# Kernel optimization log

Measured on AMD Instinct MI355X. Metric: run time of the kernel, lower is better.

The kernel has to match this reference:

```python
import jax, jax.numpy as jnp
import numpy as np

EPS = 1e-12  # matches torch F.normalize default eps
KERNEL_NUM = 128
SUPPORT_NUM = 7


def _knn_exclude_self(x, k):
    # x: (bs, n, d) -> (bs, n, k) indices of k nearest neighbors (self excluded)
    inner = jnp.einsum('bnd,bmd->bnm', x, x)
    q = jnp.sum(x * x, axis=2)
    dist = -2.0 * inner + q[:, None, :] + q[:, :, None]
    _, idx = jax.lax.top_k(-dist, k + 1)  # smallest distances
    return idx[:, :, 1:]


def _gather_neighbors(t, idx):
    # t: (bs, n, c), idx: (bs, n, k) -> (bs, n, k, c)
    return jax.vmap(lambda tb, ib: tb[ib])(t, idx)


def setup_inputs() -> dict:
    key = jax.random.key(0)
    k1, k2, k3, k4 = jax.random.split(key, 4)
    bs, n = 2, 8192
    stdv = 1.0 / np.sqrt(SUPPORT_NUM * KERNEL_NUM)
    return {
        'vertices': jax.random.normal(k1, (bs, n, 3), dtype=jnp.float32),
        'directions': jax.random.uniform(k2, (3, SUPPORT_NUM * KERNEL_NUM), dtype=jnp.float32, minval=-stdv, maxval=stdv),
        'W_ste': jax.random.normal(k3, (KERNEL_NUM, 3), dtype=jnp.float32) * (1.0 / np.sqrt(3.0)),
        'W_conv2': jax.random.normal(k4, (KERNEL_NUM, 2 * KERNEL_NUM), dtype=jnp.float32) * (1.0 / np.sqrt(2.0 * KERNEL_NUM)),
        'neighbor_num': 16,
    }


def reference(vertices, directions, W_ste, W_conv2, neighbor_num):
    bs, n, _ = vertices.shape
    kernel_num = W_ste.shape[0]
    support_num = directions.shape[1] // kernel_num

    # STE branch: 1x1 conv over channels (3 -> kernel_num)
    f_ste = jnp.einsum('bnd,kd->bnk', vertices, W_ste)

    # receptive fields (RF-P): kNN in point space, normalized directions
    idx = _knn_exclude_self(vertices, neighbor_num)  # (bs, n, K)
    nbrs = _gather_neighbors(vertices, idx)          # (bs, n, K, 3)
    dirvec = nbrs - vertices[:, :, None, :]
    dir_norm = dirvec / jnp.maximum(jnp.linalg.norm(dirvec, axis=-1, keepdims=True), EPS)

    # graph conv
    sup = directions / jnp.maximum(jnp.linalg.norm(directions, axis=0, keepdims=True), EPS)
    theta = jax.nn.relu(jnp.einsum('bnkd,ds->bnks', dir_norm, sup))
    theta = theta.reshape(bs, n, neighbor_num, support_num, kernel_num)
    feature = jnp.mean(jnp.max(theta, axis=2), axis=2)  # (bs, n, kernel_num)

    # ORL: global pooling over kNN-maxed features (same point-space kNN indices)
    nb_feat = jnp.max(_gather_neighbors(feature, idx), axis=2)   # (bs, n, kernel_num)
    f_global = jnp.broadcast_to(jnp.mean(nb_feat, axis=1, keepdims=True), feature.shape)
    feat_cat = jnp.concatenate([feature, f_global], axis=-1)     # (bs, n, 2*kernel_num)
    feature = jnp.einsum('bnc,kc->bnk', feat_cat, W_conv2) + feature

    return feature + f_ste
```

## Files before the change

kernel.cpp:

```cpp
#include <hip/hip_runtime.h>
#include <math.h>

#define N     8192
#define BS    2
#define KNN   16
#define SUP   7
#define KC    128
#define SK    (SUP*KC)
#define NCH   32
#define CH    (N/NCH)
#define SLOTS 12
#define CAP   (NCH*SLOTS)
#define QG    256
#define PPB   16
#define OPB   8
#define LCAP  96
#define LSTR  98

typedef unsigned long long ull;
typedef unsigned short ushort4v __attribute__((ext_vector_type(4)));

__device__ __forceinline__ float dist2(float4 a, float4 b) {
    float dx = a.x - b.x, dy = a.y - b.y, dz = a.z - b.z;
    return fmaf(dx, dx, fmaf(dy, dy, dz * dz));
}

#define SW(Kt) { ull _lo = (Kt < _n) ? Kt : _n; ull _hi = (Kt < _n) ? _n : Kt; Kt = _lo; _n = _hi; }
#define INS16(NK) do { ull _n = (NK); if (_n < K15) { \
    SW(K0) SW(K1) SW(K2) SW(K3) SW(K4) SW(K5) SW(K6) SW(K7) \
    SW(K8) SW(K9) SW(K10) SW(K11) SW(K12) SW(K13) SW(K14) SW(K15) } } while(0)

#define DECL16 ull K0=~0ull,K1=~0ull,K2=~0ull,K3=~0ull,K4=~0ull,K5=~0ull,K6=~0ull,K7=~0ull, \
                   K8=~0ull,K9=~0ull,K10=~0ull,K11=~0ull,K12=~0ull,K13=~0ull,K14=~0ull,K15=~0ull;

__global__ void k_prep(const float* __restrict__ verts, const float* __restrict__ dirs,
                       const float* __restrict__ wste, const float* __restrict__ wconv,
                       float4* __restrict__ vb4, float4* __restrict__ sup4,
                       float4* __restrict__ wste4, float4* __restrict__ wt4) {
    int t = blockIdx.x * blockDim.x + threadIdx.x;
    if (t < BS * N) {
        float x = verts[t*3], y = verts[t*3+1], z = verts[t*3+2];
        vb4[t] = make_float4(x, y, z, 0.5f * fmaf(x, x, fmaf(y, y, z*z)));
    }
    int u = t - BS * N;
    if (u >= 0 && u < SK) {
        float x = dirs[u], y = dirs[SK + u], z = dirs[2*SK + u];
        float inv = 1.f / fmaxf(sqrtf(fmaf(x, x, fmaf(y, y, z*z))), 1e-12f);
        sup4[u] = make_float4(x*inv, y*inv, z*inv, 0.f);
    }
    int v = u - SK;
    if (v >= 0 && v < KC)
        wste4[v] = make_float4(wste[v*3], wste[v*3+1], wste[v*3+2], 0.f);
    int w = v - KC;
    if (w >= 0 && w < 32*KC) {
        int c4 = w >> 7, k = w & 127;
        const float* r = wconv + k*2*KC + c4*4;
        wt4[w] = make_float4(r[0], r[1], r[2], r[3]);
    }
}

__global__ void k_thr(const float4* __restrict__ vb4, float* __restrict__ thr) {
    __shared__ float4 SB[2048];
    __shared__ float4 SA[512];
    int b = blockIdx.y;
    int tid = threadIdx.x;
    const float4* vb = vb4 + b * N;
#pragma unroll
    for (int s = 0; s < 8; ++s)
        SB[tid + 256*s] = vb[tid + 256*s];
    __syncthreads();
#pragma unroll
    for (int s = 0; s < 2; ++s) {
        int t = tid + 256*s;
        SA[t] = SB[4*t];
    }
    __syncthreads();
    int sub = tid & 7;
    int i = blockIdx.x * 32 + (tid >> 3);
    float4 q = vb[i];
    float b0 = 3.4e38f, b1 = 3.4e38f, b2 = 3.4e38f, b3 = 3.4e38f;
#pragma unroll 8
    for (int s = 0; s < 64; ++s) {
        int t = s * 8 + sub;
        float d = dist2(q, SA[t]);
        if (4*t == i) d = 3.4e38f;
        float t0 = fminf(b0, d); float r = fmaxf(b0, d); b0 = t0;
        float t1 = fminf(b1, r); r = fmaxf(b1, r); b1 = t1;
        float t2 = fminf(b2, r); r = fmaxf(b2, r); b2 = t2;
        b3 = fminf(b3, r);
    }
#pragma unroll
    for (int st = 1; st < 8; st <<= 1) {
        float c0 = __shfl_xor(b0, st, 64);
        float c1 = __shfl_xor(b1, st, 64);
        float c2 = __shfl_xor(b2, st, 64);
        float c3 = __shfl_xor(b3, st, 64);
        float m0 = fminf(b0, c3), m1 = fminf(b1, c2);
        float m2 = fminf(b2, c1), m3 = fminf(b3, c0);
        float x0 = fminf(m0, m2), x2 = fmaxf(m0, m2);
        float x1 = fminf(m1, m3), x3 = fmaxf(m1, m3);
        b0 = fminf(x0, x1); b1 = fmaxf(x0, x1);
        b2 = fminf(x2, x3); b3 = fmaxf(x2, x3);
    }
    float t4 = b3;
    int c = 0;
#pragma unroll 8
    for (int s = 0; s < 256; ++s) {
        int p = s * 8 + sub;
        float d = dist2(q, SB[p]);
        c += (d <= t4 && p != i) ? 1 : 0;
    }
    c += __shfl_xor(c, 1, 64);
    c += __shfl_xor(c, 2, 64);
    c += __shfl_xor(c, 4, 64);
    if (sub == 0) {
        float f = __powf(12.0f / (float)c, 0.3333333f);
        thr[b*N + i] = t4 * f;
    }
}

__global__ void k_append(const float4* __restrict__ vb4, const float* __restrict__ thr,
                         int* __restrict__ ccnt, unsigned short* __restrict__ cand) {
    int b = blockIdx.z, qg = blockIdx.x, c = blockIdx.y;
    const float4* vb = vb4 + b * N;
    int base = c * CH;
    int i = qg * QG + threadIdx.x;
    int qi = b*N + i;
    float4 q = vb[i];
    float h = q.w - 0.5f * thr[qi];
    unsigned short* mycand = cand + ((size_t)qi * NCH + c) * SLOTS;
    const float4* pts = vb + base;
    int p = 0;
#pragma unroll 8
    for (int j = 0; j < CH; ++j) {
        float4 pt = pts[j];
        float lhs = fmaf(q.x, pt.x, fmaf(q.y, pt.y, fmaf(q.z, pt.z, -pt.w)));
        if (lhs >= h) {
            mycand[p < SLOTS ? p : SLOTS-1] = (unsigned short)(base + j);
            p++;
        }
    }
    ccnt[qi * NCH + c] = p;
}

#define GRP4W(CP, SOFF) { \
    ushort4v gv = *(const ushort4v*)((CP) + (SOFF)); \
    int jj[4]; \
    _Pragma("unroll") for (int s = 0; s < 4; ++s) jj[s] = (int)gv[s]; \
    float4 pv[4]; \
    _Pragma("unroll") for (int s = 0; s < 4; ++s) pv[s] = vb[jj[s] & (N-1)]; \
    _Pragma("unroll") for (int s = 0; s < 4; ++s) { \
        if ((SOFF + s) < nc) { \
            float d = dist2(q, pv[s]); \
            lkeys[kb + off + SOFF + s] = ((ull)__float_as_uint(d) << 32) | (unsigned)jj[s]; \
        } \
    } }

__global__ void k_select(const float4* __restrict__ vb4, const int* __restrict__ ccnt,
                         const unsigned short* __restrict__ cand, int* __restrict__ idxout,
                         int* __restrict__ fbcnt, int* __restrict__ fblist) {
    __shared__ ull lkeys[32 * LSTR];
    int b = blockIdx.y;
    int tid = threadIdx.x;
    int sub = tid & 7;
    int ql = tid >> 3;
    int i = blockIdx.x * 32 + ql;
    int qi = b*N + i;
    int kb = ql * LSTR;
    int c0 = 4*sub;

    int total = 0, mx = 0, off0 = 0;
#pragma unroll
    for (int c4 = 0; c4 < NCH/4; ++c4) {
        int4 v = *(const int4*)(ccnt + qi*NCH + c4*4);
        total += v.x + v.y + v.z + v.w;
        mx = max(mx, max(max(v.x, v.y), max(v.z, v.w)));
        int bb = c4*4;
        off0 += (bb+0 < c0 ? v.x : 0) + (bb+1 < c0 ? v.y : 0)
              + (bb+2 < c0 ? v.z : 0) + (bb+3 < c0 ? v.w : 0);
    }
    bool bad = (total < KNN + 1) || (mx > SLOTS) || (total > LCAP);
    if (bad && sub == 0) {
        int p = atomicAdd(fbcnt, 1);
        fblist[p] = qi;
    }

    const float4* vb = vb4 + b * N;
    float4 q = vb[i];
    if (!bad) {
        const unsigned short* mycand = cand + (size_t)qi * CAP;
        int off = off0;
#pragma unroll
        for (int u = 0; u < 4; ++u) {
            int c = c0 + u;
            int nc = ccnt[qi * NCH + c];
            const unsigned short* cp = mycand + c * SLOTS;
            if (nc > 0) {
                GRP4W(cp, 0);
                if (nc > 4) {
                    GRP4W(cp, 4);
                    if (nc > 8) GRP4W(cp, 8);
                }
            }
            off += nc;
        }
    }
    __syncthreads();
    if (bad) return;

    ull kp[12];
#pragma unroll
    for (int t = 0; t < 12; ++t) {
        int p = sub + 8*t;
        kp[t] = (p < total) ? lkeys[kb + p] : ~0ull;
    }
    int rank[12];
#pragma unroll
    for (int t = 0; t < 12; ++t) rank[t] = 0;
    for (int j = 0; j < total; ++j) {
        ull kj = lkeys[kb + j];
#pragma unroll
        for (int t = 0; t < 12; ++t)
            rank[t] += (kj < kp[t]) ? 1 : 0;
    }
    int* oi = idxout + (size_t)qi * KNN;
#pragma unroll
    for (int t = 0; t < 12; ++t)
        if (rank[t] >= 1 && rank[t] <= KNN)
            oi[rank[t]-1] = (int)(kp[t] & 0xffffffffu);
}

__global__ void k_fallback(const float4* __restrict__ vb4, const int* __restrict__ fbcnt,
                           const int* __restrict__ fblist, int* __restrict__ idxout) {
    __shared__ ull heap[16*256];
    int nfb = *fbcnt;
    int tid = threadIdx.x;
    int lane = tid & 63, wv = tid >> 6;
    for (int w = blockIdx.x; w < nfb; w += gridDim.x) {
        int qi = fblist[w];
        int b = qi >> 13, i = qi & (N-1);
        const float4* vb = vb4 + b * N;
        float4 q = vb[i];
        DECL16;
        for (int s = 0; s < N/256; ++s) {
            int j = tid + s*256;
            if (j == i) continue;
            float d = dist2(q, vb[j]);
            ull nk = ((ull)__float_as_uint(d) << 32) | (unsigned)j;
            INS16(nk);
        }
        heap[0*256+tid]=K0;   heap[1*256+tid]=K1;   heap[2*256+tid]=K2;   heap[3*256+tid]=K3;
        heap[4*256+tid]=K4;   heap[5*256+tid]=K5;   heap[6*256+tid]=K6;   heap[7*256+tid]=K7;
        heap[8*256+tid]=K8;   heap[9*256+tid]=K9;   heap[10*256+tid]=K10; heap[11*256+tid]=K11;
        heap[12*256+tid]=K12; heap[13*256+tid]=K13; heap[14*256+tid]=K14; heap[15*256+tid]=K15;
        __syncthreads();
        if (wv == 0) {
            int l0 = lane*4, l1 = lane*4+1, l2 = lane*4+2, l3 = lane*4+3;
            int p0 = 0, p1 = 0, p2 = 0, p3 = 0;
            int* oi = idxout + (size_t)qi * KNN;
            for (int r = 0; r < KNN; ++r) {
                ull h0 = (p0 < 16) ? heap[p0*256 + l0] : ~0ull;
                ull h1 = (p1 < 16) ? heap[p1*256 + l1] : ~0ull;
                ull h2 = (p2 < 16) ? heap[p2*256 + l2] : ~0ull;
                ull h3 = (p3 < 16) ? heap[p3*256 + l3] : ~0ull;
                ull a01 = h0 < h1 ? h0 : h1;
                ull a23 = h2 < h3 ? h2 : h3;
                ull h   = a01 < a23 ? a01 : a23;
                ull m = h;
#pragma unroll
                for (int s = 1; s < 64; s <<= 1) {
                    ull o = __shfl_xor(m, s, 64);
                    m = (o < m) ? o : m;
                }
                if (h == m && m != ~0ull) {
                    if      (h0 == m) p0++;
                    else if (h1 == m) p1++;
                    else if (h2 == m) p2++;
                    else              p3++;
                }
                if (lane == r) oi[r] = (int)(m & 0xffffffffu);
            }
        }
        __syncthreads();
    }
}

__global__ void k_feature(const float4* __restrict__ vb4, const float4* __restrict__ sup4,
                          const int* __restrict__ idx, float* __restrict__ feat) {
    int b = blockIdx.y, i = blockIdx.x;
    __shared__ float4 dirn[KNN];
    const float4* vb = vb4 + b * N;
    if (threadIdx.x < KNN) {
        int j = idx[(size_t)(b*N + i)*KNN + threadIdx.x];
        float4 q = vb[i], p = vb[j];
        float dx = p.x - q.x, dy = p.y - q.y, dz = p.z - q.z;
        float inv = 1.f / fmaxf(sqrtf(fmaf(dx, dx, fmaf(dy, dy, dz*dz))), 1e-12f);
        dirn[threadIdx.x] = make_float4(dx*inv, dy*inv, dz*inv, 0.f);
    }
    __syncthreads();
    int k = threadIdx.x;
    float acc = 0.f;
#pragma unroll
    for (int s = 0; s < SUP; ++s) {
        float4 sv = sup4[s*KC + k];
        float m = 0.f;
#pragma unroll
        for (int K = 0; K < KNN; ++K) {
            float4 dn = dirn[K];
            float t = fmaf(dn.x, sv.x, fmaf(dn.y, sv.y, dn.z*sv.z));
            m = fmaxf(m, t);
        }
        acc += m;
    }
    feat[(size_t)(b*N + i)*KC + k] = acc * (1.f/SUP);
}

__global__ void k_nbmax(const float* __restrict__ feat, const int* __restrict__ idx,
                        float* __restrict__ partial) {
    int b = blockIdx.y;
    int p0 = blockIdx.x * PPB;
    int k = threadIdx.x;
    const float* fb = feat + (size_t)b*N*KC;
    float sum = 0.f;
    for (int p = 0; p < PPB; ++p) {
        const int* ii = idx + (size_t)(b*N + p0 + p) * KNN;
        float m = -3.4e38f;
#pragma unroll
        for (int K = 0; K < KNN; ++K)
            m = fmaxf(m, fb[(size_t)ii[K]*KC + k]);
        sum += m;
    }
    partial[(size_t)(b*(N/PPB) + blockIdx.x)*KC + k] = sum;
}

__global__ void k_global(const float* __restrict__ partial, const float* __restrict__ wconv,
                         float* __restrict__ gconst) {
    int b = blockIdx.x, k = threadIdx.x;
    float s = 0.f;
    for (int q = 0; q < N/PPB; ++q) s += partial[(size_t)(b*(N/PPB) + q)*KC + k];
    __shared__ float fg[KC];
    fg[k] = s * (1.f/N);
    __syncthreads();
    float acc = 0.f;
    for (int c = 0; c < KC; ++c)
        acc = fmaf(fg[c], wconv[k*2*KC + KC + c], acc);
    gconst[b*KC + k] = acc;
}

__global__ void k_out(const float* __restrict__ feat, const float4* __restrict__ wt4,
                      const float4* __restrict__ wste4, const float4* __restrict__ vb4,
                      const float* __restrict__ gconst, float* __restrict__ out) {
    int p0 = blockIdx.x * OPB;
    int k = threadIdx.x;
    float acc[OPB];
#pragma unroll
    for (int p = 0; p < OPB; ++p) acc[p] = 0.f;
#pragma unroll 4
    for (int c4 = 0; c4 < KC/4; ++c4) {
        float4 w = wt4[c4*KC + k];
#pragma unroll
        for (int p = 0; p < OPB; ++p) {
            const float4 f = *(const float4*)(feat + (size_t)(p0 + p)*KC + c4*4);
            acc[p] = fmaf(f.x, w.x, fmaf(f.y, w.y, fmaf(f.z, w.z, fmaf(f.w, w.w, acc[p]))));
        }
    }
    float4 ws = wste4[k];
#pragma unroll
    for (int p = 0; p < OPB; ++p) {
        int pt = p0 + p;
        int b = pt >> 13;
        float4 v = vb4[pt];
        float fste = fmaf(v.x, ws.x, fmaf(v.y, ws.y, v.z*ws.z));
        out[(size_t)pt*KC + k] = acc[p] + gconst[b*KC + k] + feat[(size_t)pt*KC + k] + fste;
    }
}

extern "C" void kernel_launch(void* const* d_in, const int* in_sizes, int n_in,
                              void* d_out, int out_size, void* d_ws, size_t ws_size,
                              hipStream_t stream) {
    const float* verts = (const float*)d_in[0];
    const float* dirs  = (const float*)d_in[1];
    const float* wste  = (const float*)d_in[2];
    const float* wconv = (const float*)d_in[3];
    float* out = (float*)d_out;

    float* ws = (float*)d_ws;
    float4* vb4   = (float4*)ws;
    float4* sup4  = vb4 + BS*N;
    float4* wste4 = sup4 + SK;
    float4* wt4   = wste4 + KC;
    float*  thr   = (float*)(wt4 + 32*KC);
    int*    ccnt  = (int*)(thr + BS*N);
    int*    fbcnt = ccnt + BS*N*NCH;
    int*    fblist= fbcnt + 16;
    unsigned short* cand = (unsigned short*)(fblist + BS*N);
    float*  feat  = (float*)cand;
    int*    idx   = (int*)(cand + (size_t)BS*N*CAP);
    float*  partial = (float*)(idx + (size_t)BS*N*KNN);
    float*  gconst  = partial + (size_t)BS*(N/PPB)*KC;

    hipMemsetAsync(fbcnt, 0, 16*sizeof(int), stream);
    k_prep<<<(BS*N + SK + KC + 32*KC + 255)/256, 256, 0, stream>>>(verts, dirs, wste, wconv,
                                                                   vb4, sup4, wste4, wt4);
    k_thr<<<dim3(N/32, BS), 256, 0, stream>>>(vb4, thr);
    k_append<<<dim3(N/QG, NCH, BS), 256, 0, stream>>>(vb4, thr, ccnt, cand);
    k_select<<<dim3(N/32, BS), 256, 0, stream>>>(vb4, ccnt, cand, idx, fbcnt, fblist);
    k_fallback<<<1024, 256, 0, stream>>>(vb4, fbcnt, fblist, idx);
    k_feature<<<dim3(N, BS), KC, 0, stream>>>(vb4, sup4, idx, feat);
    k_nbmax<<<dim3(N/PPB, BS), KC, 0, stream>>>(feat, idx, partial);
    k_global<<<BS, KC, 0, stream>>>(partial, wconv, gconst);
    k_out<<<BS*N/OPB, KC, 0, stream>>>(feat, wt4, wste4, vb4, gconst, out);
}
```

Baseline: 188.7 us.

## Fuse candidate append and select into one shared-memory kNN kernel

Replaces the two-pass kNN candidate scheme (per-chunk global candidate slots plus a separate select kernel) with a single kernel. It stages points in LDS in 2048-point chunks, filters them against the per-query threshold, and appends candidate keys directly into LDS through a per-query atomic counter. This removes the global candidate and count buffers, one launch, and the scattered gathers of candidate vertices. In exchange, each block now scans all N points, where before one thread per query scanned a chunk, and it relies on LDS atomics whose ordering is nondeterministic. The rank-based selection makes the result order-independent.

```diff
diff --git a/kernel.cpp b/kernel.cpp
--- a/kernel.cpp
+++ b/kernel.cpp
@@ -7,18 +7,12 @@
 #define SUP   7
 #define KC    128
 #define SK    (SUP*KC)
-#define NCH   32
-#define CH    (N/NCH)
-#define SLOTS 12
-#define CAP   (NCH*SLOTS)
-#define QG    256
 #define PPB   16
 #define OPB   8
 #define LCAP  96
 #define LSTR  98
 
 typedef unsigned long long ull;
-typedef unsigned short ushort4v __attribute__((ext_vector_type(4)));
 
 __device__ __forceinline__ float dist2(float4 a, float4 b) {
     float dx = a.x - b.x, dy = a.y - b.y, dz = a.z - b.z;
@@ -119,47 +113,12 @@
     }
 }
 
-__global__ void k_append(const float4* __restrict__ vb4, const float* __restrict__ thr,
-                         int* __restrict__ ccnt, unsigned short* __restrict__ cand) {
-    int b = blockIdx.z, qg = blockIdx.x, c = blockIdx.y;
-    const float4* vb = vb4 + b * N;
-    int base = c * CH;
-    int i = qg * QG + threadIdx.x;
-    int qi = b*N + i;
-    float4 q = vb[i];
-    float h = q.w - 0.5f * thr[qi];
-    unsigned short* mycand = cand + ((size_t)qi * NCH + c) * SLOTS;
-    const float4* pts = vb + base;
-    int p = 0;
-#pragma unroll 8
-    for (int j = 0; j < CH; ++j) {
-        float4 pt = pts[j];
-        float lhs = fmaf(q.x, pt.x, fmaf(q.y, pt.y, fmaf(q.z, pt.z, -pt.w)));
-        if (lhs >= h) {
-            mycand[p < SLOTS ? p : SLOTS-1] = (unsigned short)(base + j);
-            p++;
-        }
-    }
-    ccnt[qi * NCH + c] = p;
-}
-
-#define GRP4W(CP, SOFF) { \
-    ushort4v gv = *(const ushort4v*)((CP) + (SOFF)); \
-    int jj[4]; \
-    _Pragma("unroll") for (int s = 0; s < 4; ++s) jj[s] = (int)gv[s]; \
-    float4 pv[4]; \
-    _Pragma("unroll") for (int s = 0; s < 4; ++s) pv[s] = vb[jj[s] & (N-1)]; \
-    _Pragma("unroll") for (int s = 0; s < 4; ++s) { \
-        if ((SOFF + s) < nc) { \
-            float d = dist2(q, pv[s]); \
-            lkeys[kb + off + SOFF + s] = ((ull)__float_as_uint(d) << 32) | (unsigned)jj[s]; \
-        } \
-    } }
-
-__global__ void k_select(const float4* __restrict__ vb4, const int* __restrict__ ccnt,
-                         const unsigned short* __restrict__ cand, int* __restrict__ idxout,
-                         int* __restrict__ fbcnt, int* __restrict__ fblist) {
+__global__ void k_knn(const float4* __restrict__ vb4, const float* __restrict__ thr,
+                      int* __restrict__ idxout, int* __restrict__ fbcnt,
+                      int* __restrict__ fblist) {
+    __shared__ float4 pts[2048];
     __shared__ ull lkeys[32 * LSTR];
+    __shared__ int lcnt[32];
     int b = blockIdx.y;
     int tid = threadIdx.x;
     int sub = tid & 7;
@@ -167,47 +126,40 @@
     int i = blockIdx.x * 32 + ql;
     int qi = b*N + i;
     int kb = ql * LSTR;
-    int c0 = 4*sub;
-
-    int total = 0, mx = 0, off0 = 0;
-#pragma unroll
-    for (int c4 = 0; c4 < NCH/4; ++c4) {
-        int4 v = *(const int4*)(ccnt + qi*NCH + c4*4);
-        total += v.x + v.y + v.z + v.w;
-        mx = max(mx, max(max(v.x, v.y), max(v.z, v.w)));
-        int bb = c4*4;
-        off0 += (bb+0 < c0 ? v.x : 0) + (bb+1 < c0 ? v.y : 0)
-              + (bb+2 < c0 ? v.z : 0) + (bb+3 < c0 ? v.w : 0);
-    }
-    bool bad = (total < KNN + 1) || (mx > SLOTS) || (total > LCAP);
-    if (bad && sub == 0) {
-        int p = atomicAdd(fbcnt, 1);
-        fblist[p] = qi;
-    }
-
     const float4* vb = vb4 + b * N;
     float4 q = vb[i];
-    if (!bad) {
-        const unsigned short* mycand = cand + (size_t)qi * CAP;
-        int off = off0;
-#pragma unroll
-        for (int u = 0; u < 4; ++u) {
-            int c = c0 + u;
-            int nc = ccnt[qi * NCH + c];
-            const unsigned short* cp = mycand + c * SLOTS;
-            if (nc > 0) {
-                GRP4W(cp, 0);
-                if (nc > 4) {
-                    GRP4W(cp, 4);
-                    if (nc > 8) GRP4W(cp, 8);
+    float h = q.w - 0.5f * thr[qi];
+    if (tid < 32) lcnt[tid] = 0;
+
+    for (int ch = 0; ch < 4; ++ch) {
+        __syncthreads();
+        int base = ch * 2048;
+#pragma unroll
+        for (int s = 0; s < 8; ++s)
+            pts[tid + 256*s] = vb[base + tid + 256*s];
+        __syncthreads();
+#pragma unroll 8
+        for (int s = 0; s < 256; ++s) {
+            int p = s * 8 + sub;
+            float4 pt = pts[p];
+            float lhs = fmaf(q.x, pt.x, fmaf(q.y, pt.y, fmaf(q.z, pt.z, -pt.w)));
+            if (lhs >= h) {
+                int pos = atomicAdd(&lcnt[ql], 1);
+                if (pos < LCAP) {
+                    float d = dist2(q, pt);
+                    lkeys[kb + pos] = ((ull)__float_as_uint(d) << 32)
+                                    | (unsigned)(base + p);
                 }
             }
-            off += nc;
-        }
-    }
-    __syncthreads();
-    if (bad) return;
-
+        }
+    }
+    __syncthreads();
+    int total = lcnt[ql];
+    bool bad = (total < KNN + 1) || (total > LCAP);
+    if (bad) {
+        if (sub == 0) { int p = atomicAdd(fbcnt, 1); fblist[p] = qi; }
+        return;
+    }
     ull kp[12];
 #pragma unroll
     for (int t = 0; t < 12; ++t) {
@@ -390,12 +342,10 @@
     float4* wste4 = sup4 + SK;
     float4* wt4   = wste4 + KC;
     float*  thr   = (float*)(wt4 + 32*KC);
-    int*    ccnt  = (int*)(thr + BS*N);
-    int*    fbcnt = ccnt + BS*N*NCH;
+    int*    fbcnt = (int*)(thr + BS*N);
     int*    fblist= fbcnt + 16;
-    unsigned short* cand = (unsigned short*)(fblist + BS*N);
-    float*  feat  = (float*)cand;
-    int*    idx   = (int*)(cand + (size_t)BS*N*CAP);
+    float*  feat  = (float*)(fblist + BS*N);
+    int*    idx   = (int*)(feat + (size_t)BS*N*KC);
     float*  partial = (float*)(idx + (size_t)BS*N*KNN);
     float*  gconst  = partial + (size_t)BS*(N/PPB)*KC;
 
@@ -403,8 +353,7 @@
     k_prep<<<(BS*N + SK + KC + 32*KC + 255)/256, 256, 0, stream>>>(verts, dirs, wste, wconv,
                                                                    vb4, sup4, wste4, wt4);
     k_thr<<<dim3(N/32, BS), 256, 0, stream>>>(vb4, thr);
-    k_append<<<dim3(N/QG, NCH, BS), 256, 0, stream>>>(vb4, thr, ccnt, cand);
-    k_select<<<dim3(N/32, BS), 256, 0, stream>>>(vb4, ccnt, cand, idx, fbcnt, fblist);
+    k_knn<<<dim3(N/32, BS), 256, 0, stream>>>(vb4, thr, idx, fbcnt, fblist);
     k_fallback<<<1024, 256, 0, stream>>>(vb4, fbcnt, fblist, idx);
     k_feature<<<dim3(N, BS), KC, 0, stream>>>(vb4, sup4, idx, feat);
     k_nbmax<<<dim3(N/PPB, BS), KC, 0, stream>>>(feat, idx, partial);
```

After: 237.1 us. 1.26x slower.
